# Kernel tuning notes

Measured on AMD Instinct MI355X. Metric: run time of the kernel, lower is better.

The kernel has to match this reference:

```python
import jax, jax.numpy as jnp
import numpy as np

B, T, D, H, TE = 4, 8192, 512, 8, 2048
Dh = D // H
EPS = 1e-5


def layer_norm(x, g, b):
    mu = jnp.mean(x, axis=-1, keepdims=True)
    var = jnp.mean(jnp.square(x - mu), axis=-1, keepdims=True)
    return (x - mu) * jax.lax.rsqrt(var + EPS) * g + b


def setup_inputs() -> dict:
    key = jax.random.key(0)
    ks = jax.random.split(key, 8)
    s = 0.02  # typical init scale
    return {
        "x": jax.random.normal(ks[0], (B, T, D), jnp.float32),
        "emb": jax.random.normal(ks[1], (B, TE), jnp.float32),
        "src_mask": (jax.random.uniform(ks[2], (B, T, 1)) > 0.2).astype(jnp.float32),
        "gamma": jnp.ones((D,), jnp.float32),
        "beta": jnp.zeros((D,), jnp.float32),
        "Wq": jax.random.normal(ks[3], (D, D), jnp.float32) * s,
        "bq": jnp.zeros((D,), jnp.float32),
        "Wk": jax.random.normal(ks[4], (D, D), jnp.float32) * s,
        "bk": jnp.zeros((D,), jnp.float32),
        "Wv": jax.random.normal(ks[5], (D, D), jnp.float32) * s,
        "bv": jnp.zeros((D,), jnp.float32),
        "emb_W": jax.random.normal(ks[6], (TE, 2 * D), jnp.float32) * s,
        "emb_b": jnp.zeros((2 * D,), jnp.float32),
        "gamma2": jnp.ones((D,), jnp.float32),
        "beta2": jnp.zeros((D,), jnp.float32),
        "out_W": jax.random.normal(ks[7], (D, D), jnp.float32) * s,
        "out_b": jnp.zeros((D,), jnp.float32),
    }


def reference(x, emb, src_mask, gamma, beta, Wq, bq, Wk, bk, Wv, bv,
              emb_W, emb_b, gamma2, beta2, out_W, out_b):
    # x: (B,T,D); emb: (B,TE); src_mask: (B,T,1)
    xn = layer_norm(x, gamma, beta)  # single LN reused (same math as 3 calls)
    q = xn @ Wq + bq
    k = xn @ Wk + bk + (1.0 - src_mask) * -1000000.0
    v = (xn @ Wv + bv) * src_mask
    q = jax.nn.softmax(q.reshape(B, T, H, Dh), axis=-1)  # softmax over head dim
    k = jax.nn.softmax(k.reshape(B, T, H, Dh), axis=1)   # softmax over time
    v = v.reshape(B, T, H, Dh)
    attn = jnp.einsum('bthd,bthl->bhdl', k, v)           # (B,H,Dh,Dh) KV state
    y = jnp.einsum('bthd,bhdl->bthl', q, attn).reshape(B, T, D)
    # StylizationBlock (dropout inactive in eval)
    emb_out = jax.nn.silu(emb) @ emb_W + emb_b           # (B, 2D)
    scale, shift = jnp.split(emb_out[:, None, :], 2, axis=2)
    h = layer_norm(y, gamma2, beta2) * (1.0 + scale) + shift
    h = jax.nn.silu(h) @ out_W + out_b
    return x + h
```

## Files before the change

### kernel.cpp

```cpp
#include <hip/hip_runtime.h>
#include <cstdint>
#include <cstddef>

typedef unsigned short u16;
typedef unsigned int u32;
typedef __attribute__((ext_vector_type(8))) short short8;
typedef __attribute__((ext_vector_type(4))) float f32x4;

static constexpr int CB = 4;
static constexpr int CT = 8192;
static constexpr int CD = 512;
static constexpr int CH = 8;
static constexpr int CDH = 64;
static constexpr int CTE = 2048;
static constexpr int CD2 = 1024;

__device__ __forceinline__ float b2f(u16 u) {
    return __uint_as_float(((u32)u) << 16);
}
__device__ __forceinline__ u16 f2b(float f) {
    u32 i = __float_as_uint(f);
    i = i + 0x7fffu + ((i >> 16) & 1u);
    return (u16)(i >> 16);
}

typedef const __attribute__((address_space(1))) void* gas_p;
typedef __attribute__((address_space(3))) void* las_p;
#define GLD16(g, l) __builtin_amdgcn_global_load_lds((gas_p)(g), (las_p)(l), 16, 0, 0)

__global__ __launch_bounds__(256) void zero_kernel(float* __restrict__ p, int n) {
    int i = blockIdx.x * 256 + threadIdx.x;
    if (i < n) p[i] = 0.0f;
}

__global__ __launch_bounds__(256) void wconv_kernel(
        const float* __restrict__ W0, const float* __restrict__ W1,
        const float* __restrict__ W2, const float* __restrict__ W3,
        u16* __restrict__ Wt)
{
    const float* W;
    switch (blockIdx.y) {
        case 0: W = W0; break;
        case 1: W = W1; break;
        case 2: W = W2; break;
        default: W = W3; break;
    }
    u16* o = Wt + (size_t)blockIdx.y * CD * CD;
    const int k0 = (blockIdx.x >> 3) * 64;
    const int n0 = (blockIdx.x & 7) * 64;
    const int tid = threadIdx.x;
    __shared__ u16 tile[64][65];
    const int nn = tid & 63, kq = tid >> 6;
#pragma unroll
    for (int i = 0; i < 16; i++) {
        const int kk = i * 4 + kq;
        tile[kk][nn] = f2b(W[(size_t)(k0 + kk) * CD + n0 + nn]);
    }
    __syncthreads();
    const int kk2 = tid & 63, nq = tid >> 6;
#pragma unroll
    for (int i = 0; i < 16; i++) {
        const int nn2 = i * 4 + nq;
        o[(size_t)(n0 + nn2) * CD + k0 + kk2] = tile[kk2][nn2];
    }
}

__global__ __launch_bounds__(256) void ln1_kernel(const float* __restrict__ x,
        const float* __restrict__ g, const float* __restrict__ bt,
        u16* __restrict__ xn)
{
    const int row = blockIdx.x;
    const int tid = threadIdx.x;
    const float2 p = ((const float2*)(x + (size_t)row * CD))[tid];
    float s = p.x + p.y;
    float sq = p.x * p.x + p.y * p.y;
#pragma unroll
    for (int m = 1; m < 64; m <<= 1) { s += __shfl_xor(s, m); sq += __shfl_xor(sq, m); }
    __shared__ float red[8];
    const int wid = tid >> 6;
    if ((tid & 63) == 0) { red[wid] = s; red[wid + 4] = sq; }
    __syncthreads();
    s = red[0] + red[1] + red[2] + red[3];
    sq = red[4] + red[5] + red[6] + red[7];
    const float mu = s * (1.0f / CD);
    float var = sq * (1.0f / CD) - mu * mu;
    var = fmaxf(var, 0.0f);
    const float rs = rsqrtf(var + 1e-5f);
    const float2 gv = ((const float2*)g)[tid];
    const float2 bv = ((const float2*)bt)[tid];
    const float y0 = (p.x - mu) * rs * gv.x + bv.x;
    const float y1 = (p.y - mu) * rs * gv.y + bv.y;
    ((u32*)(xn + (size_t)row * CD))[tid] = (u32)f2b(y0) | ((u32)f2b(y1) << 16);
}

__global__ __launch_bounds__(512, 1) void gemm_mfma(
    const u16* __restrict__ A, const u16* __restrict__ Bt,
    const float* __restrict__ bias, const float* __restrict__ bias2,
    void* __restrict__ Cv, void* __restrict__ Cv2,
    const float* __restrict__ mask, const float* __restrict__ xres,
    int mode)
{
    __shared__ u16 SH[2][512][32];
    const int tid = threadIdx.x;
    const int wave = tid >> 6, lane = tid & 63;
    const int quad = lane >> 4, l16 = lane & 15;

    const int n = blockIdx.x;
    const int xcd = n & 7;
    int by, bx;
    if (mode == 4) { const int slot = n >> 3; by = xcd * 16 + (slot >> 2); bx = slot & 3; }
    else           { const int slot = n >> 3; by = xcd * 16 + (slot >> 1); bx = slot & 1; }
    const int row0 = by * 256;
    const int col0 = bx * 256;
    const int wm = (wave >> 2) * 128;
    const int wn = (wave & 3) * 64;

    int emode = mode;
    const float* bptr = bias;
    void* cout = Cv;
    int ocol0 = col0;
    if (mode == 4) {
        if (col0 >= 512) { emode = 2; bptr = bias2; cout = Cv2; ocol0 = col0 - 512; }
        else emode = 1;
    }

    f32x4 acc[8][4];
#pragma unroll
    for (int mt = 0; mt < 8; mt++)
#pragma unroll
        for (int nt = 0; nt < 4; nt++)
            acc[mt][nt] = (f32x4){0.0f, 0.0f, 0.0f, 0.0f};

    const int srow = lane >> 2;
    const int sslot = lane & 3;
    const int swz = (srow >> 1) & 3;
    const int aw0 = wave * 32;
    const u16* gA0 = A + (size_t)(row0 + aw0 + srow) * CD + (sslot ^ swz) * 8;
    const u16* gA1 = gA0 + (size_t)16 * CD;
    const u16* gB0 = Bt + (size_t)(col0 + aw0 + srow) * CD + (sslot ^ swz) * 8;
    const u16* gB1 = gB0 + (size_t)16 * CD;

#define STAGE_T(bf, kt) do { \
        GLD16(gA0 + (kt) * 32, &SH[bf][aw0][0]); \
        GLD16(gA1 + (kt) * 32, &SH[bf][aw0 + 16][0]); \
        GLD16(gB0 + (kt) * 32, &SH[bf][256 + aw0][0]); \
        GLD16(gB1 + (kt) * 32, &SH[bf][256 + aw0 + 16][0]); \
    } while (0)

    STAGE_T(0, 0);

    const int swsel = (quad ^ ((l16 >> 1) & 3)) * 8;

#pragma unroll
    for (int t = 0; t < 16; ++t) {
        const int bf = t & 1;
        if (t < 15) STAGE_T(bf ^ 1, t + 1);
        if (t < 15) asm volatile("s_waitcnt vmcnt(4)\ns_barrier" ::: "memory");
        else        asm volatile("s_waitcnt vmcnt(0)\ns_barrier" ::: "memory");

        short8 bfr[4];
#pragma unroll
        for (int nt = 0; nt < 4; nt++)
            bfr[nt] = *(const short8*)&SH[bf][256 + wn + nt * 16 + l16][swsel];
        __builtin_amdgcn_s_setprio(1);
#pragma unroll
        for (int mt = 0; mt < 8; mt++) {
            const short8 af = *(const short8*)&SH[bf][wm + mt * 16 + l16][swsel];
#pragma unroll
            for (int nt = 0; nt < 4; nt++)
                acc[mt][nt] = __builtin_amdgcn_mfma_f32_16x16x32_bf16(
                    af, bfr[nt], acc[mt][nt], 0, 0, 0);
        }
        __builtin_amdgcn_s_setprio(0);
        asm volatile("s_waitcnt lgkmcnt(0)\ns_barrier" ::: "memory");
    }
#undef STAGE_T

    if (emode == 3) {
#pragma unroll
        for (int mt = 0; mt < 8; mt++) {
            const int rbase = row0 + wm + mt * 16 + quad * 4;
#pragma unroll
            for (int r = 0; r < 4; r++) {
                const int row = rbase + r;
#pragma unroll
                for (int nt = 0; nt < 4; nt++) {
                    const int col = ocol0 + wn + nt * 16 + l16;
                    const float val = acc[mt][nt][r] + bptr[col];
                    ((float*)cout)[(size_t)row * CD + col] =
                        val + xres[(size_t)row * CD + col];
                }
            }
        }
    } else {
        float* stg = ((float*)&SH[0][0][0]) + wave * 1040;
#pragma unroll
        for (int mt = 0; mt < 8; mt++) {
#pragma unroll
            for (int r = 0; r < 4; r++) {
                const int rr = quad * 4 + r;
                const int grow = row0 + wm + mt * 16 + rr;
                float mval = 0.0f;
                if (emode == 1 || emode == 2) mval = mask[grow];
#pragma unroll
                for (int nt = 0; nt < 4; nt++) {
                    const int ocol = ocol0 + wn + nt * 16 + l16;
                    float val = acc[mt][nt][r] + bptr[ocol];
                    if (emode == 1) val += (1.0f - mval) * -1000000.0f;
                    else if (emode == 2) val *= mval;
                    stg[rr * 65 + nt * 16 + l16] = val;
                }
            }
            u16* cbase = (u16*)cout + (size_t)(row0 + wm + mt * 16) * CD + ocol0 + wn;
#pragma unroll
            for (int i = 0; i < 8; i++) {
                const int rr = i * 2 + (lane >> 5);
                const int c2 = lane & 31;
                const float f0 = stg[rr * 65 + 2 * c2];
                const float f1 = stg[rr * 65 + 2 * c2 + 1];
                ((u32*)(cbase + (size_t)rr * CD))[c2] =
                    (u32)f2b(f0) | ((u32)f2b(f1) << 16);
            }
        }
    }
}

__global__ __launch_bounds__(256) void ksm_partial(const u16* __restrict__ k,
        float* __restrict__ pm, float* __restrict__ ps)
{
    const int bid = blockIdx.x;
    const int b = bid >> 5, ch = bid & 31;
    const int tid = threadIdx.x;
    const u32* base = (const u32*)(k + (size_t)b * CT * CD + (size_t)ch * 256 * CD) + tid;
    float m0 = -3.0e38f, m1 = -3.0e38f;
#pragma unroll 8
    for (int r = 0; r < 256; ++r) {
        const u32 p = base[(size_t)r * 256];
        m0 = fmaxf(m0, b2f((u16)(p & 0xffff)));
        m1 = fmaxf(m1, b2f((u16)(p >> 16)));
    }
    float s0 = 0.0f, s1 = 0.0f;
#pragma unroll 8
    for (int r = 0; r < 256; ++r) {
        const u32 p = base[(size_t)r * 256];
        s0 += __expf(b2f((u16)(p & 0xffff)) - m0);
        s1 += __expf(b2f((u16)(p >> 16)) - m1);
    }
    const int d0 = tid * 2;
    pm[((size_t)b * CD + d0) * 32 + ch] = m0;
    pm[((size_t)b * CD + d0 + 1) * 32 + ch] = m1;
    ps[((size_t)b * CD + d0) * 32 + ch] = s0;
    ps[((size_t)b * CD + d0 + 1) * 32 + ch] = s1;
}

__global__ __launch_bounds__(256) void ksm_norm(u16* __restrict__ k,
        const float* __restrict__ pm, const float* __restrict__ ps)
{
    const int bid = blockIdx.x;
    const int b = bid >> 5, ch = bid & 31;
    const int tid = threadIdx.x;
    const int d0 = tid * 2;
    const float* pm0 = pm + ((size_t)b * CD + d0) * 32;
    const float* pm1 = pm0 + 32;
    const float* ps0 = ps + ((size_t)b * CD + d0) * 32;
    const float* ps1 = ps0 + 32;
    float M0 = -3.0e38f, M1 = -3.0e38f;
#pragma unroll
    for (int c = 0; c < 32; ++c) { M0 = fmaxf(M0, pm0[c]); M1 = fmaxf(M1, pm1[c]); }
    float S0 = 0.0f, S1 = 0.0f;
#pragma unroll
    for (int c = 0; c < 32; ++c) {
        S0 += ps0[c] * __expf(pm0[c] - M0);
        S1 += ps1[c] * __expf(pm1[c] - M1);
    }
    const float R0 = 1.0f / S0, R1 = 1.0f / S1;
    u32* base = (u32*)(k + (size_t)b * CT * CD + (size_t)ch * 256 * CD) + tid;
#pragma unroll 4
    for (int r = 0; r < 256; ++r) {
        const u32 p = base[(size_t)r * 256];
        const float x0 = __expf(b2f((u16)(p & 0xffff)) - M0) * R0;
        const float x1 = __expf(b2f((u16)(p >> 16)) - M1) * R1;
        base[(size_t)r * 256] = (u32)f2b(x0) | ((u32)f2b(x1) << 16);
    }
}

__global__ __launch_bounds__(256) void attn_kernel(const u16* __restrict__ k,
        const u16* __restrict__ v, float* __restrict__ attn)
{
    const int bid = blockIdx.x;
    const int bh = bid >> 4, ch = bid & 15;
    const int b = bh >> 3, h = bh & 7;
    const int tid = threadIdx.x;
    __shared__ u16 Ks[32][64], Vs[32][64];
    const int ti = tid >> 4, tj = tid & 15;
    const int d0 = ti * 4, l0 = tj * 4;
    const int trow = tid >> 3, cg8 = (tid & 7) * 8;
    float acc[4][4];
#pragma unroll
    for (int r = 0; r < 4; r++)
#pragma unroll
        for (int c = 0; c < 4; c++) acc[r][c] = 0.0f;

    for (int st = 0; st < 16; st++) {
        const int t0 = ch * 512 + st * 32;
        const size_t goff = ((size_t)(b * CT + t0 + trow)) * CD + h * 64 + cg8;
        const uint4 kv4 = *(const uint4*)(k + goff);
        const uint4 vv4 = *(const uint4*)(v + goff);
        __syncthreads();
        *(uint4*)&Ks[trow][cg8] = kv4;
        *(uint4*)&Vs[trow][cg8] = vv4;
        __syncthreads();
#pragma unroll
        for (int tt = 0; tt < 32; tt++) {
            const ushort4 ka = *(const ushort4*)&Ks[tt][d0];
            const ushort4 va = *(const ushort4*)&Vs[tt][l0];
            const float kr[4] = { b2f(ka.x), b2f(ka.y), b2f(ka.z), b2f(ka.w) };
            const float vr[4] = { b2f(va.x), b2f(va.y), b2f(va.z), b2f(va.w) };
#pragma unroll
            for (int r = 0; r < 4; r++)
#pragma unroll
                for (int c = 0; c < 4; c++)
                    acc[r][c] = fmaf(kr[r], vr[c], acc[r][c]);
        }
    }
    float* ab = attn + (size_t)bh * 64 * 64;
#pragma unroll
    for (int r = 0; r < 4; r++)
#pragma unroll
        for (int c = 0; c < 4; c++)
            atomicAdd(&ab[(d0 + r) * 64 + l0 + c], acc[r][c]);
}

__global__ __launch_bounds__(256) void y_mfma(const u16* __restrict__ q,
        const float* __restrict__ attn, u16* __restrict__ y)
{
    const int bid = blockIdx.x;
    const int bh = bid >> 5;
    const int chunk = bid & 31;
    const int b = bh >> 3, h = bh & 7;
    const int tid = threadIdx.x;
    const int wave = tid >> 6, lane = tid & 63;
    const int quad = lane >> 4, l16 = lane & 15;

    __shared__ u16 Bh[64][72];
    __shared__ u16 Bl[64][72];
    __shared__ float Ys[4][16][65];

    const float* ab = attn + (size_t)bh * 64 * 64;
#pragma unroll
    for (int i = 0; i < 16; i++) {
        const int idx = i * 256 + tid;
        const int d = idx >> 6, l = idx & 63;
        const float a = ab[idx];
        const u16 hi = f2b(a);
        Bh[l][d] = hi;
        Bl[l][d] = f2b(a - b2f(hi));
    }
    __syncthreads();

    short8 bhf[4][2], blf[4][2];
#pragma unroll
    for (int nt = 0; nt < 4; nt++)
#pragma unroll
        for (int ks = 0; ks < 2; ks++) {
            bhf[nt][ks] = *(const short8*)&Bh[nt * 16 + l16][ks * 32 + quad * 8];
            blf[nt][ks] = *(const short8*)&Bl[nt * 16 + l16][ks * 32 + quad * 8];
        }

    const int rowbase = chunk * 256 + wave * 64;
    const size_t qb = ((size_t)(b * CT + rowbase)) * CD + h * 64;

#pragma unroll
    for (int it = 0; it < 4; it++) {
        const u16* qp = q + qb + (size_t)(it * 16 + l16) * CD + quad * 8;
        const uint4 q0 = *(const uint4*)qp;
        const uint4 q1 = *(const uint4*)(qp + 32);
        float xv[16];
        const u32 qw[8] = { q0.x, q0.y, q0.z, q0.w, q1.x, q1.y, q1.z, q1.w };
#pragma unroll
        for (int j = 0; j < 8; j++) {
            xv[2 * j]     = b2f((u16)(qw[j] & 0xffff));
            xv[2 * j + 1] = b2f((u16)(qw[j] >> 16));
        }
        float m = xv[0];
#pragma unroll
        for (int j = 1; j < 16; j++) m = fmaxf(m, xv[j]);
        m = fmaxf(m, __shfl_xor(m, 16));
        m = fmaxf(m, __shfl_xor(m, 32));
        float s = 0.0f;
#pragma unroll
        for (int j = 0; j < 16; j++) { xv[j] = __expf(xv[j] - m); s += xv[j]; }
        s += __shfl_xor(s, 16);
        s += __shfl_xor(s, 32);
        const float rinv = 1.0f / s;
        short8 ah[2], al[2];
#pragma unroll
        for (int ks = 0; ks < 2; ks++)
#pragma unroll
            for (int j = 0; j < 8; j++) {
                const float v = xv[ks * 8 + j] * rinv;
                const u16 hi = f2b(v);
                ah[ks][j] = (short)hi;
                al[ks][j] = (short)f2b(v - b2f(hi));
            }

        f32x4 acc[4];
#pragma unroll
        for (int nt = 0; nt < 4; nt++) acc[nt] = (f32x4){0.f, 0.f, 0.f, 0.f};
#pragma unroll
        for (int nt = 0; nt < 4; nt++) {
            acc[nt] = __builtin_amdgcn_mfma_f32_16x16x32_bf16(ah[0], bhf[nt][0], acc[nt], 0, 0, 0);
            acc[nt] = __builtin_amdgcn_mfma_f32_16x16x32_bf16(ah[1], bhf[nt][1], acc[nt], 0, 0, 0);
            acc[nt] = __builtin_amdgcn_mfma_f32_16x16x32_bf16(ah[0], blf[nt][0], acc[nt], 0, 0, 0);
            acc[nt] = __builtin_amdgcn_mfma_f32_16x16x32_bf16(ah[1], blf[nt][1], acc[nt], 0, 0, 0);
            acc[nt] = __builtin_amdgcn_mfma_f32_16x16x32_bf16(al[0], bhf[nt][0], acc[nt], 0, 0, 0);
            acc[nt] = __builtin_amdgcn_mfma_f32_16x16x32_bf16(al[1], bhf[nt][1], acc[nt], 0, 0, 0);
        }

#pragma unroll
        for (int nt = 0; nt < 4; nt++)
#pragma unroll
            for (int rr = 0; rr < 4; rr++)
                Ys[wave][quad * 4 + rr][nt * 16 + l16] = acc[nt][rr];
        u32* yo = (u32*)y + ((size_t)(b * CT + rowbase + it * 16)) * (CD / 2) + h * 32;
#pragma unroll
        for (int p = 0; p < 8; p++) {
            const int idx = p * 64 + lane;
            const int row = idx >> 5, c2 = idx & 31;
            const float f0 = Ys[wave][row][2 * c2];
            const float f1 = Ys[wave][row][2 * c2 + 1];
            yo[(size_t)row * (CD / 2) + c2] = (u32)f2b(f0) | ((u32)f2b(f1) << 16);
        }
    }
}

__global__ __launch_bounds__(256) void embsilu_kernel(const float* __restrict__ emb,
        float* __restrict__ se)
{
    const int i = blockIdx.x * 256 + threadIdx.x;
    if (i < CB * CTE) {
        const float e = emb[i];
        se[i] = e / (1.0f + __expf(-e));
    }
}
__global__ __launch_bounds__(256) void eoinit_kernel(const float* __restrict__ embB,
        float* __restrict__ eo)
{
    const int i = blockIdx.x * 256 + threadIdx.x;
    if (i < CB * CD2) eo[i] = embB[i & (CD2 - 1)];
}
__global__ __launch_bounds__(256) void embout2_kernel(const float* __restrict__ se,
        const float* __restrict__ embW, float* __restrict__ eo)
{
    const int jg = blockIdx.x & 15, kc = blockIdx.x >> 4;
    const int tid = threadIdx.x;
    const int jl = tid & 63, kgrp = tid >> 6;
    const int j = jg * 64 + jl;
    const int kbase = kc * 256 + kgrp * 64;
    const float* W = embW + (size_t)kbase * CD2 + j;
    const float* s0 = se + kbase;
    const float* s1 = s0 + CTE;
    const float* s2 = s1 + CTE;
    const float* s3 = s2 + CTE;
    float a0 = 0.0f, a1 = 0.0f, a2 = 0.0f, a3 = 0.0f;
#pragma unroll 8
    for (int kk = 0; kk < 64; kk++) {
        const float w = W[(size_t)kk * CD2];
        a0 = fmaf(s0[kk], w, a0);
        a1 = fmaf(s1[kk], w, a1);
        a2 = fmaf(s2[kk], w, a2);
        a3 = fmaf(s3[kk], w, a3);
    }
    __shared__ float red[4][4][64];
    red[kgrp][0][jl] = a0; red[kgrp][1][jl] = a1;
    red[kgrp][2][jl] = a2; red[kgrp][3][jl] = a3;
    __syncthreads();
    if (tid < 64) {
#pragma unroll
        for (int b = 0; b < 4; b++) {
            const float t = red[0][b][tid] + red[1][b][tid]
                          + red[2][b][tid] + red[3][b][tid];
            atomicAdd(&eo[(size_t)b * CD2 + jg * 64 + tid], t);
        }
    }
}

__global__ __launch_bounds__(256) void ln2_style_kernel(const u16* __restrict__ y,
        const float* __restrict__ g2, const float* __restrict__ bt2,
        const float* __restrict__ eo, u16* __restrict__ sout)
{
    const int row = blockIdx.x;
    const int tid = threadIdx.x;
    const int b = row >> 13;
    const u32 p = ((const u32*)(y + (size_t)row * CD))[tid];
    const float x0 = b2f((u16)(p & 0xffff));
    const float x1 = b2f((u16)(p >> 16));
    float s = x0 + x1;
    float sq = x0 * x0 + x1 * x1;
#pragma unroll
    for (int m = 1; m < 64; m <<= 1) { s += __shfl_xor(s, m); sq += __shfl_xor(sq, m); }
    __shared__ float red[8];
    const int wid = tid >> 6;
    if ((tid & 63) == 0) { red[wid] = s; red[wid + 4] = sq; }
    __syncthreads();
    s = red[0] + red[1] + red[2] + red[3];
    sq = red[4] + red[5] + red[6] + red[7];
    const float mu = s * (1.0f / CD);
    float var = sq * (1.0f / CD) - mu * mu;
    var = fmaxf(var, 0.0f);
    const float rs = rsqrtf(var + 1e-5f);
    const float2 gv = ((const float2*)g2)[tid];
    const float2 bv = ((const float2*)bt2)[tid];
    const float2 sc = ((const float2*)(eo + (size_t)b * CD2))[tid];
    const float2 sh = ((const float2*)(eo + (size_t)b * CD2 + CD))[tid];
    float h0 = (x0 - mu) * rs * gv.x + bv.x;
    float h1 = (x1 - mu) * rs * gv.y + bv.y;
    h0 = h0 * (1.0f + sc.x) + sh.x;
    h1 = h1 * (1.0f + sc.y) + sh.y;
    const float s0 = h0 / (1.0f + __expf(-h0));
    const float s1 = h1 / (1.0f + __expf(-h1));
    ((u32*)(sout + (size_t)row * CD))[tid] = (u32)f2b(s0) | ((u32)f2b(s1) << 16);
}

extern "C" void kernel_launch(void* const* d_in, const int* in_sizes, int n_in,
                              void* d_out, int out_size, void* d_ws, size_t ws_size,
                              hipStream_t stream) {
    (void)in_sizes; (void)n_in; (void)out_size; (void)ws_size;
    const float* x    = (const float*)d_in[0];
    const float* emb  = (const float*)d_in[1];
    const float* mask = (const float*)d_in[2];
    const float* gamma= (const float*)d_in[3];
    const float* beta = (const float*)d_in[4];
    const float* Wq   = (const float*)d_in[5];
    const float* bq   = (const float*)d_in[6];
    const float* Wk   = (const float*)d_in[7];
    const float* bk   = (const float*)d_in[8];
    const float* Wv   = (const float*)d_in[9];
    const float* bv   = (const float*)d_in[10];
    const float* embW = (const float*)d_in[11];
    const float* embB = (const float*)d_in[12];
    const float* g2   = (const float*)d_in[13];
    const float* bt2  = (const float*)d_in[14];
    const float* outW = (const float*)d_in[15];
    const float* outb = (const float*)d_in[16];

    char* od = (char*)d_out;
    u16* kq  = (u16*)od;
    u16* vy  = (u16*)(od + 33554432);
    float* outp = (float*)d_out;

    char* ws = (char*)d_ws;
    u16* xn   = (u16*)ws;
    u16* WtK  = (u16*)(ws + 33554432);
    u16* WtV  = WtK + (size_t)CD * CD;
    u16* WtQ  = WtV + (size_t)CD * CD;
    u16* WtO  = WtQ + (size_t)CD * CD;
    float* pm   = (float*)(ws + 35651584);
    float* ps   = (float*)(ws + 35651584 + 262144);
    float* attn = (float*)(ws + 35651584);
    float* eo   = (float*)(ws + 36306944);
    float* se   = (float*)(ws + 36323328);

    wconv_kernel<<<dim3(64, 4), 256, 0, stream>>>(Wk, Wv, Wq, outW, WtK);
    ln1_kernel<<<CB * CT, 256, 0, stream>>>(x, gamma, beta, xn);
    embsilu_kernel<<<32, 256, 0, stream>>>(emb, se);
    eoinit_kernel<<<16, 256, 0, stream>>>(embB, eo);
    embout2_kernel<<<128, 256, 0, stream>>>(se, embW, eo);
    gemm_mfma<<<512, 512, 0, stream>>>(xn, WtK, bk, bv, kq, vy, mask, nullptr, 4);
    ksm_partial<<<128, 256, 0, stream>>>(kq, pm, ps);
    ksm_norm<<<128, 256, 0, stream>>>(kq, pm, ps);
    zero_kernel<<<512, 256, 0, stream>>>(attn, CB * CH * CDH * CDH);
    attn_kernel<<<512, 256, 0, stream>>>(kq, vy, attn);
    gemm_mfma<<<256, 512, 0, stream>>>(xn, WtQ, bq, nullptr, kq, nullptr, nullptr, nullptr, 0);
    y_mfma<<<1024, 256, 0, stream>>>(kq, attn, vy);
    ln2_style_kernel<<<CB * CT, 256, 0, stream>>>(vy, g2, bt2, eo, xn );
    gemm_mfma<<<256, 512, 0, stream>>>(xn , WtO, outb, nullptr, outp, nullptr, nullptr, x, 3);
}
```

Baseline: 452.2 us.

## Compute K^T V state with bf16 MFMA and double-buffered async loads

The scalar-FMA attn_kernel, which built each head's 64x64 KV state, is replaced by attn_mfma. Each wave now streams its own 128-row slice of K and V into LDS through double-buffered direct global-to-LDS loads. It reads transposed fragments with ds_read_b64_tr_b16 and accumulates with 16x16x32 bf16 MFMA instructions. The four wave partials are reduced in LDS before a single set of atomicAdds per block, so each block issues a quarter as many global atomics. This moves the reduction over time onto the matrix cores, at the cost of a more complex kernel that relies on inline-asm wait counts.

```diff
diff --git a/kernel.cpp b/kernel.cpp
--- a/kernel.cpp
+++ b/kernel.cpp
@@ -5,6 +5,7 @@
 typedef unsigned short u16;
 typedef unsigned int u32;
 typedef __attribute__((ext_vector_type(8))) short short8;
+typedef __attribute__((ext_vector_type(4))) short short4v;
 typedef __attribute__((ext_vector_type(4))) float f32x4;
 
 static constexpr int CB = 4;
@@ -284,51 +285,103 @@
     }
 }
 
-__global__ __launch_bounds__(256) void attn_kernel(const u16* __restrict__ k,
+__global__ __launch_bounds__(256) void attn_mfma(const u16* __restrict__ k,
         const u16* __restrict__ v, float* __restrict__ attn)
 {
     const int bid = blockIdx.x;
     const int bh = bid >> 4, ch = bid & 15;
     const int b = bh >> 3, h = bh & 7;
     const int tid = threadIdx.x;
-    __shared__ u16 Ks[32][64], Vs[32][64];
-    const int ti = tid >> 4, tj = tid & 15;
-    const int d0 = ti * 4, l0 = tj * 4;
-    const int trow = tid >> 3, cg8 = (tid & 7) * 8;
-    float acc[4][4];
-#pragma unroll
-    for (int r = 0; r < 4; r++)
-#pragma unroll
-        for (int c = 0; c < 4; c++) acc[r][c] = 0.0f;
-
-    for (int st = 0; st < 16; st++) {
-        const int t0 = ch * 512 + st * 32;
-        const size_t goff = ((size_t)(b * CT + t0 + trow)) * CD + h * 64 + cg8;
-        const uint4 kv4 = *(const uint4*)(k + goff);
-        const uint4 vv4 = *(const uint4*)(v + goff);
-        __syncthreads();
-        *(uint4*)&Ks[trow][cg8] = kv4;
-        *(uint4*)&Vs[trow][cg8] = vv4;
-        __syncthreads();
-#pragma unroll
-        for (int tt = 0; tt < 32; tt++) {
-            const ushort4 ka = *(const ushort4*)&Ks[tt][d0];
-            const ushort4 va = *(const ushort4*)&Vs[tt][l0];
-            const float kr[4] = { b2f(ka.x), b2f(ka.y), b2f(ka.z), b2f(ka.w) };
-            const float vr[4] = { b2f(va.x), b2f(va.y), b2f(va.z), b2f(va.w) };
+    const int wave = tid >> 6, lane = tid & 63;
+    const int quad = lane >> 4, l16 = lane & 15;
+
+    __shared__ u16 SH[4][2][2][2048];
+
+    f32x4 acc[4][4];
+#pragma unroll
+    for (int mt = 0; mt < 4; mt++)
+#pragma unroll
+        for (int nt = 0; nt < 4; nt++)
+            acc[mt][nt] = (f32x4){0.0f, 0.0f, 0.0f, 0.0f};
+
+    const size_t rb = (size_t)(b * CT + ch * 512 + wave * 128 + (lane >> 1)) * CD
+                    + h * 64 + (lane & 1) * 8;
+    const u16* gk = k + rb;
+    const u16* gv = v + rb;
+
+#define ASTAGE(bf, i) do { \
+        const size_t o_ = (size_t)(i) * 32 * CD; \
+        GLD16(gk + o_,      &SH[wave][bf][0][0]); \
+        GLD16(gk + o_ + 16, &SH[wave][bf][0][512]); \
+        GLD16(gk + o_ + 32, &SH[wave][bf][0][1024]); \
+        GLD16(gk + o_ + 48, &SH[wave][bf][0][1536]); \
+        GLD16(gv + o_,      &SH[wave][bf][1][0]); \
+        GLD16(gv + o_ + 16, &SH[wave][bf][1][512]); \
+        GLD16(gv + o_ + 32, &SH[wave][bf][1][1024]); \
+        GLD16(gv + o_ + 48, &SH[wave][bf][1][1536]); \
+    } while (0)
+
+    ASTAGE(0, 0);
+
+    const u32 lbase = (u32)(uintptr_t)(las_p)&SH[wave][0][0][0];
+    const u32 atr = lbase + quad * 256 + l16 * 8;
+
+    for (int i = 0; i < 4; ++i) {
+        const int bf = i & 1;
+        if (i < 3) {
+            ASTAGE(bf ^ 1, i + 1);
+            asm volatile("s_waitcnt vmcnt(8)" ::: "memory");
+        } else {
+            asm volatile("s_waitcnt vmcnt(0)" ::: "memory");
+        }
+        const u32 ak = atr + bf * 8192;
+        const u32 av = ak + 4096;
+        short4v kh0[4], kh1[4], vh0[4], vh1[4];
+#pragma unroll
+        for (int db = 0; db < 4; db++) {
+            asm volatile("ds_read_b64_tr_b16 %0, %2 offset:0\n\t"
+                         "ds_read_b64_tr_b16 %1, %2 offset:128"
+                         : "=&v"(kh0[db]), "=&v"(kh1[db])
+                         : "v"(ak + db * 1024));
+            asm volatile("ds_read_b64_tr_b16 %0, %2 offset:0\n\t"
+                         "ds_read_b64_tr_b16 %1, %2 offset:128"
+                         : "=&v"(vh0[db]), "=&v"(vh1[db])
+                         : "v"(av + db * 1024));
+        }
+        asm volatile("s_waitcnt lgkmcnt(0)" ::: "memory");
+        __builtin_amdgcn_sched_barrier(0);
+        short8 kf[4], vf[4];
+#pragma unroll
+        for (int db = 0; db < 4; db++) {
+            kf[db] = __builtin_shufflevector(kh0[db], kh1[db], 0, 1, 2, 3, 4, 5, 6, 7);
+            vf[db] = __builtin_shufflevector(vh0[db], vh1[db], 0, 1, 2, 3, 4, 5, 6, 7);
+        }
+#pragma unroll
+        for (int mt = 0; mt < 4; mt++)
+#pragma unroll
+            for (int nt = 0; nt < 4; nt++)
+                acc[mt][nt] = __builtin_amdgcn_mfma_f32_16x16x32_bf16(
+                    kf[mt], vf[nt], acc[mt][nt], 0, 0, 0);
+    }
+#undef ASTAGE
+
+    float* Cw = (float*)&SH[wave][0][0][0];
+#pragma unroll
+    for (int mt = 0; mt < 4; mt++)
+#pragma unroll
+        for (int nt = 0; nt < 4; nt++)
 #pragma unroll
             for (int r = 0; r < 4; r++)
-#pragma unroll
-                for (int c = 0; c < 4; c++)
-                    acc[r][c] = fmaf(kr[r], vr[c], acc[r][c]);
-        }
-    }
-    float* ab = attn + (size_t)bh * 64 * 64;
-#pragma unroll
-    for (int r = 0; r < 4; r++)
-#pragma unroll
-        for (int c = 0; c < 4; c++)
-            atomicAdd(&ab[(d0 + r) * 64 + l0 + c], acc[r][c]);
+                Cw[(mt * 16 + quad * 4 + r) * 64 + nt * 16 + l16] = acc[mt][nt][r];
+    __syncthreads();
+    const float* C0 = (const float*)&SH[0][0][0][0];
+    float* ab = attn + (size_t)bh * 4096;
+#pragma unroll
+    for (int i = 0; i < 16; i++) {
+        const int idx = i * 256 + tid;
+        atomicAdd(&ab[idx],
+                  C0[idx] + C0[idx + 4096] + C0[idx + 8192] + C0[idx + 12288]);
+    }
 }
 
 __global__ __launch_bounds__(256) void y_mfma(const u16* __restrict__ q,
@@ -570,7 +623,7 @@
     ksm_partial<<<128, 256, 0, stream>>>(kq, pm, ps);
     ksm_norm<<<128, 256, 0, stream>>>(kq, pm, ps);
     zero_kernel<<<512, 256, 0, stream>>>(attn, CB * CH * CDH * CDH);
-    attn_kernel<<<512, 256, 0, stream>>>(kq, vy, attn);
+    attn_mfma<<<512, 256, 0, stream>>>(kq, vy, attn);
     gemm_mfma<<<256, 512, 0, stream>>>(xn, WtQ, bq, nullptr, kq, nullptr, nullptr, nullptr, 0);
     y_mfma<<<1024, 256, 0, stream>>>(kq, attn, vy);
     ln2_style_kernel<<<CB * CT, 256, 0, stream>>>(vy, g2, bt2, eo, xn );
```

Measured after the change: 412.5 us. 8.8% less time.
